# Kernel tuning notes

Measured on AMD Instinct MI355X. Metric: run time of the kernel, lower is better.

Reference implementation:

```python
import jax, jax.numpy as jnp
import numpy as np

B, L, D_IN, D_OUT = 4, 1024, 2048, 2048
H, G = 32, 8            # num_heads, num_kv_groups
HD = D_OUT // H         # head_dim = 64
R = H // G              # group_size = 4


def setup_inputs() -> dict:
    key = jax.random.key(0)
    ks = jax.random.split(key, 7)
    s = 0.02
    return {
        "query": jax.random.normal(ks[0], (B, L, D_IN), jnp.float32),
        "key": jax.random.normal(ks[1], (B, L, D_IN), jnp.float32),
        "value": jax.random.normal(ks[2], (B, L, D_IN), jnp.float32),
        "Wq": jax.random.normal(ks[3], (D_IN, D_OUT), jnp.float32) * s,
        "Wk": jax.random.normal(ks[4], (D_IN, G * HD), jnp.float32) * s,
        "Wv": jax.random.normal(ks[5], (D_IN, G * HD), jnp.float32) * s,
        "Wo": jax.random.normal(ks[6], (D_OUT, D_OUT), jnp.float32) * s,
        # causal mask: positions where mask==True are set to -inf (original uses attn_mask == 1)
        "attn_mask": jnp.triu(jnp.ones((L, L), dtype=bool), k=1),
    }


def reference(query, key, value, Wq, Wk, Wv, Wo, attn_mask):
    b, t, _ = query.shape
    # projections (Linear, no bias)
    q = (query @ Wq).reshape(b, t, G, R, HD)      # head h = g*R + r matches repeat_interleave ordering
    k = (key @ Wk).reshape(b, -1, G, HD)
    v = (value @ Wv).reshape(b, -1, G, HD)
    # NOTE: original code applies NO 1/sqrt(head_dim) scaling — kept faithful.
    # scores: (b, g, r, t, s); KV broadcast over r instead of repeat_interleave
    scores = jnp.einsum('btgrd,bsgd->bgrts', q, k)
    scores = jnp.where(attn_mask[None, None, None, :, :], -jnp.inf, scores)
    weights = jax.nn.softmax(scores, axis=-1)     # dropout p=0.0 -> identity
    ctx = jnp.einsum('bgrts,bsgd->btgrd', weights, v).reshape(b, t, D_OUT)
    attn_output = ctx @ Wo
    attn_output_weights = weights.reshape(b * H, t, -1)  # (b n) t s
    return attn_output, attn_output_weights
```

## Files before the change

### kernel.cpp

```cpp
#include <hip/hip_runtime.h>
#include <math.h>

typedef _Float16 f16;
typedef __attribute__((ext_vector_type(8))) _Float16 f16x8;
typedef __attribute__((ext_vector_type(4))) _Float16 f16x4;
typedef __attribute__((ext_vector_type(4))) float f32x4;
typedef unsigned int u32;

#define MFMA16(a, b, c) __builtin_amdgcn_mfma_f32_16x16x32_f16(a, b, c, 0, 0, 0)

__device__ __forceinline__ void gload16(const void* g, void* l) {
  __builtin_amdgcn_global_load_lds((const __attribute__((address_space(1))) u32*)g,
                                   (__attribute__((address_space(3))) u32*)l, 16, 0, 0);
}

__global__ __launch_bounds__(256) void prep_kernel(
    const float* __restrict__ q, const float* __restrict__ k, const float* __restrict__ v,
    f16* __restrict__ qh, f16* __restrict__ kh, f16* __restrict__ vh,
    const float* __restrict__ Wq, const float* __restrict__ Wk,
    const float* __restrict__ Wv, const float* __restrict__ Wo,
    f16* __restrict__ WqT, f16* __restrict__ WkT,
    f16* __restrict__ WvT, f16* __restrict__ WoT) {
  __shared__ f16 tile[64][66];
  const int bx = blockIdx.x;
  const int t = threadIdx.x;
  if (bx < 24576) {
    const int sel = bx >> 13;
    const float* in = (sel == 0) ? q : (sel == 1) ? k : v;
    f16* out = (sel == 0) ? qh : (sel == 1) ? kh : vh;
    const int i = (bx & 8191) * 1024 + t * 4;
    float4 vv = *(const float4*)(in + i);
    f16x4 h;
    h[0] = (f16)vv.x; h[1] = (f16)vv.y; h[2] = (f16)vv.z; h[3] = (f16)vv.w;
    *(f16x4*)(out + i) = h;
    return;
  }
  int id = bx - 24576;
  const float* in;
  f16* out;
  int K, N;
  if (id < 1024)      { in = Wq; out = WqT; K = 2048; N = 2048; }
  else if (id < 1280) { in = Wk; out = WkT; K = 2048; N = 512;  id -= 1024; }
  else if (id < 1536) { in = Wv; out = WvT; K = 2048; N = 512;  id -= 1280; }
  else                { in = Wo; out = WoT; K = 2048; N = 2048; id -= 1536; }
  const int ntn = N >> 6;
  const int tk = (id / ntn) * 64, tn = (id % ntn) * 64;
#pragma unroll
  for (int i = 0; i < 16; i++) {
    int idx = i * 256 + t;
    int r = idx >> 6, c = idx & 63;
    tile[c][r] = (f16)in[(size_t)(tk + r) * N + tn + c];
  }
  __syncthreads();
#pragma unroll
  for (int i = 0; i < 16; i++) {
    int idx = i * 256 + t;
    int r = idx >> 6, c = idx & 63;
    out[(size_t)(tn + r) * K + tk + c] = tile[r][c];
  }
}

template <bool F32OUT>
__device__ __forceinline__ void gemm_body(const f16* __restrict__ Ap,
                                          const f16* __restrict__ Btp,
                                          void* __restrict__ Cp,
                                          int m0, int n0, int N, int K, int vmode) {
  const int tid = threadIdx.x, lane = tid & 63, wid = tid >> 6;
  const int lg = lane >> 4, lr = lane & 15;
  const int wr = (wid >> 1) << 6, wc = (wid & 1) << 6;
  __shared__ f16 As[2][128 * 64];
  __shared__ f16 Bs[2][128 * 64];
  auto stage = [&](const f16* Gp, f16* Ls, int row0, int k0) {
#pragma unroll
    for (int c = 0; c < 4; c++) {
      int u = c * 256 + tid;
      int row = u >> 3, slot = u & 7;
      int gs = slot ^ (row & 7);
      gload16(Gp + (size_t)(row0 + row) * K + k0 + gs * 8,
              Ls + (c * 256 + wid * 64) * 8);
    }
  };
  f32x4 acc[4][4] = {};
  const int nk = K >> 6;
  stage(Ap, As[0], m0, 0);
  stage(Btp, Bs[0], n0, 0);
  for (int k = 0; k < nk; k++) {
    const int cb = k & 1;
    __builtin_amdgcn_s_barrier();
    __builtin_amdgcn_sched_barrier(0);
    if (k + 1 < nk) {
      stage(Ap, As[cb ^ 1], m0, (k + 1) << 6);
      stage(Btp, Bs[cb ^ 1], n0, (k + 1) << 6);
      __builtin_amdgcn_sched_barrier(0);
      asm volatile("s_waitcnt vmcnt(8)" ::: "memory");
    } else {
      __builtin_amdgcn_sched_barrier(0);
      asm volatile("s_waitcnt vmcnt(0)" ::: "memory");
    }
    __builtin_amdgcn_s_barrier();
    __builtin_amdgcn_sched_barrier(0);
    asm volatile("" ::: "memory");
#pragma unroll
    for (int kk = 0; kk < 2; kk++) {
      f16x8 af[4], bf[4];
#pragma unroll
      for (int i = 0; i < 4; i++) {
        int row = wr + i * 16 + lr;
        int sl = (kk * 4 + lg) ^ (row & 7);
        af[i] = *(const f16x8*)&As[cb][row * 64 + sl * 8];
      }
#pragma unroll
      for (int i = 0; i < 4; i++) {
        int row = wc + i * 16 + lr;
        int sl = (kk * 4 + lg) ^ (row & 7);
        bf[i] = *(const f16x8*)&Bs[cb][row * 64 + sl * 8];
      }
#pragma unroll
      for (int i = 0; i < 4; i++)
#pragma unroll
        for (int j = 0; j < 4; j++)
          acc[i][j] = MFMA16(af[i], bf[j], acc[i][j]);
    }
  }
  if (F32OUT) {
    float* C = (float*)Cp;
#pragma unroll
    for (int i = 0; i < 4; i++)
#pragma unroll
      for (int j = 0; j < 4; j++)
#pragma unroll
        for (int rg = 0; rg < 4; rg++) {
          int row = m0 + wr + i * 16 + lg * 4 + rg;
          int col = n0 + wc + j * 16 + lr;
          C[(size_t)row * N + col] = acc[i][j][rg];
        }
  } else if (vmode) {
    f16* C = (f16*)Cp;
#pragma unroll
    for (int i = 0; i < 4; i++)
#pragma unroll
      for (int j = 0; j < 4; j++)
#pragma unroll
        for (int rg = 0; rg < 4; rg++) {
          int row = m0 + wr + i * 16 + lg * 4 + rg;
          int col = n0 + wc + j * 16 + lr;
          C[((size_t)(row >> 10) * 512 + col) * 1024 + (row & 1023)] = (f16)acc[i][j][rg];
        }
  } else {
    f16* C = (f16*)Cp;
#pragma unroll
    for (int i = 0; i < 4; i++)
#pragma unroll
      for (int j = 0; j < 4; j++)
#pragma unroll
        for (int rg = 0; rg < 4; rg++) {
          int row = m0 + wr + i * 16 + lg * 4 + rg;
          int col = n0 + wc + j * 16 + lr;
          C[(size_t)row * N + col] = (f16)acc[i][j][rg];
        }
  }
}

__global__ __launch_bounds__(256) void gemm_proj(
    const f16* __restrict__ qh, const f16* __restrict__ WqT, f16* __restrict__ Qp,
    const f16* __restrict__ kh, const f16* __restrict__ WkT, f16* __restrict__ Kpj,
    const f16* __restrict__ vh, const f16* __restrict__ WvT, f16* __restrict__ VTp,
    float* __restrict__ wout) {
  const int bx = blockIdx.x;
  const int grp = bx / 5, rem = bx % 5;
  if (rem >= 3) {
    const int zid = grp * 2 + (rem - 3);
#pragma unroll
    for (int ci = 0; ci < 4; ci++) {
      const int c = zid * 4 + ci;
      const int bh = c >> 4, k = c & 15;
      if (k == 15) continue;
      const int cols0 = (k + 1) << 6;
      const int nc4 = (1024 - cols0) >> 2;
      float* base = wout + (size_t)bh * 1024 * 1024 + (size_t)(k << 6) * 1024 + cols0;
      f32x4 z = {};
      for (int r = 0; r < 64; r++) {
        float* rp = base + (size_t)r * 1024;
        for (int c4 = (int)threadIdx.x; c4 < nc4; c4 += 256)
          __builtin_nontemporal_store(z, (f32x4*)(rp + c4 * 4));
      }
    }
    return;
  }
  const int gid = grp * 3 + rem;
  const f16 *Ap, *Btp;
  f16* Cp;
  int N, nsh, vmode, tile;
  if (gid < 512)      { Ap = qh; Btp = WqT; Cp = Qp;  N = 2048; nsh = 4; vmode = 0; tile = gid; }
  else if (gid < 640) { Ap = kh; Btp = WkT; Cp = Kpj; N = 512;  nsh = 2; vmode = 0; tile = gid - 512; }
  else                { Ap = vh; Btp = WvT; Cp = VTp; N = 512;  nsh = 2; vmode = 1; tile = gid - 640; }
  const int m0 = (tile >> nsh) << 7, n0 = (tile & ((1 << nsh) - 1)) << 7;
  gemm_body<false>(Ap, Btp, (void*)Cp, m0, n0, N, 2048, vmode);
}

__global__ __launch_bounds__(256) void gemm_out(
    const f16* __restrict__ Ap, const f16* __restrict__ Btp, float* __restrict__ Cp) {
  const int tile = blockIdx.x;
  const int m0 = (tile >> 4) << 7, n0 = (tile & 15) << 7;
  gemm_body<true>(Ap, Btp, (void*)Cp, m0, n0, 2048, 2048, 0);
}

__global__ __launch_bounds__(256) void attn_kernel(
    const f16* __restrict__ Qp, const f16* __restrict__ Kp, const f16* __restrict__ VTp,
    float* __restrict__ Wout, f16* __restrict__ Ctx) {
  __shared__ f16 Kt[2][64 * 64];
  __shared__ f16 Vt[2][64 * 64];
  __shared__ f16 Wt[4][32 * 64];
  const int bx = (blockIdx.x & 7) * 128 + (blockIdx.x >> 3);
  const int qt = bx & 31, g = (bx >> 5) & 7, b = bx >> 8;
  const int tid = threadIdx.x, lane = tid & 63, wid = tid >> 6;
  const int lg = lane >> 4, lr = lane & 15;
  const int h = g * 4 + wid;
  const int q0 = qt * 32;
  const int st_max = (q0 + 31) >> 6;
  const float S0 = 12.0f;

  f16x8 aq[2][2];
#pragma unroll
  for (int mi = 0; mi < 2; mi++)
#pragma unroll
    for (int kk = 0; kk < 2; kk++)
      aq[mi][kk] = *(const f16x8*)(Qp + (size_t)(b * 1024 + q0 + mi * 16 + lr) * 2048 +
                                   h * 64 + kk * 32 + lg * 8);

  float l_[2][4] = {};

  auto stageK = [&](int st, int buf) {
#pragma unroll
    for (int c = 0; c < 2; c++) {
      int u = c * 256 + tid;
      int row = u >> 3, slot = u & 7;
      int gs = slot ^ (row & 7);
      gload16(Kp + (size_t)(b * 1024 + st * 64 + row) * 512 + g * 64 + gs * 8,
              &Kt[buf][(c * 256 + wid * 64) * 8]);
    }
  };
  auto stageV = [&](int st, int buf) {
#pragma unroll
    for (int c = 0; c < 2; c++) {
      int u = c * 256 + tid;
      int row = u >> 3, slot = u & 7;
      int gs = slot ^ (row & 7);
      gload16(VTp + ((size_t)b * 512 + g * 64 + row) * 1024 + st * 64 + gs * 8,
              &Vt[buf][(c * 256 + wid * 64) * 8]);
    }
  };

  int cur = 0;
  stageK(0, 0);
  for (int st = 0; st <= st_max; st++) {
    __syncthreads();
    if (st < st_max) {
      stageK(st + 1, cur ^ 1);
    } else {
      stageK(0, cur ^ 1);
      stageV(0, cur ^ 1);
    }
    f16x8 bk[4][2];
#pragma unroll
    for (int ni = 0; ni < 4; ni++)
#pragma unroll
      for (int kk = 0; kk < 2; kk++) {
        int row = ni * 16 + lr;
        int sl = (kk * 4 + lg) ^ (row & 7);
        bk[ni][kk] = *(const f16x8*)&Kt[cur][row * 64 + sl * 8];
      }
#pragma unroll
    for (int mi = 0; mi < 2; mi++) {
      f32x4 s[4];
#pragma unroll
      for (int ni = 0; ni < 4; ni++) {
        f32x4 z = {};
        z = MFMA16(aq[mi][0], bk[ni][0], z);
        z = MFMA16(aq[mi][1], bk[ni][1], z);
        s[ni] = z;
      }
      if (st == st_max) {
#pragma unroll
        for (int ni = 0; ni < 4; ni++)
#pragma unroll
          for (int rg = 0; rg < 4; rg++)
            if (st * 64 + ni * 16 + lr > q0 + mi * 16 + lg * 4 + rg) s[ni][rg] = -INFINITY;
      }
#pragma unroll
      for (int rg = 0; rg < 4; rg++) {
        float rs = __expf(s[0][rg] - S0) + __expf(s[1][rg] - S0) +
                   __expf(s[2][rg] - S0) + __expf(s[3][rg] - S0);
        rs += __shfl_xor(rs, 1);
        rs += __shfl_xor(rs, 2);
        rs += __shfl_xor(rs, 4);
        rs += __shfl_xor(rs, 8);
        l_[mi][rg] += rs;
      }
    }
    cur ^= 1;
  }
#pragma unroll
  for (int i = 0; i < 2; i++)
#pragma unroll
    for (int j = 0; j < 4; j++) l_[i][j] = 1.0f / l_[i][j];

  f32x4 o[2][4] = {};
  for (int st = 0; st <= st_max; st++) {
    __syncthreads();
    if (st < st_max) {
      stageK(st + 1, cur ^ 1);
      stageV(st + 1, cur ^ 1);
    }
    f16x8 bk[4][2];
#pragma unroll
    for (int ni = 0; ni < 4; ni++)
#pragma unroll
      for (int kk = 0; kk < 2; kk++) {
        int row = ni * 16 + lr;
        int sl = (kk * 4 + lg) ^ (row & 7);
        bk[ni][kk] = *(const f16x8*)&Kt[cur][row * 64 + sl * 8];
      }
#pragma unroll
    for (int mi = 0; mi < 2; mi++) {
#pragma unroll
      for (int ni = 0; ni < 4; ni++) {
        f32x4 z = {};
        z = MFMA16(aq[mi][0], bk[ni][0], z);
        z = MFMA16(aq[mi][1], bk[ni][1], z);
#pragma unroll
        for (int rg = 0; rg < 4; rg++) {
          float sv = z[rg];
          if (st == st_max && (st * 64 + ni * 16 + lr > q0 + mi * 16 + lg * 4 + rg))
            sv = -INFINITY;
          float w = __expf(sv - S0) * l_[mi][rg];
          int rowl = mi * 16 + lg * 4 + rg;
          __builtin_nontemporal_store(
              w, &Wout[((size_t)(b * 32 + h) * 1024 + q0 + rowl) * 1024 +
                       st * 64 + ni * 16 + lr]);
          int sl2 = (2 * ni + (lr >> 3)) ^ (rowl & 7);
          Wt[wid][rowl * 64 + sl2 * 8 + (lr & 7)] = (f16)w;
        }
      }
    }
#pragma unroll
    for (int kk = 0; kk < 2; kk++) {
      f16x8 aw[2], bv[4];
#pragma unroll
      for (int i = 0; i < 2; i++) {
        int rw = i * 16 + lr;
        int sl = (kk * 4 + lg) ^ (rw & 7);
        aw[i] = *(const f16x8*)&Wt[wid][rw * 64 + sl * 8];
      }
#pragma unroll
      for (int j = 0; j < 4; j++) {
        int rv = j * 16 + lr;
        int sl = (kk * 4 + lg) ^ (rv & 7);
        bv[j] = *(const f16x8*)&Vt[cur][rv * 64 + sl * 8];
      }
#pragma unroll
      for (int i = 0; i < 2; i++)
#pragma unroll
        for (int j = 0; j < 4; j++)
          o[i][j] = MFMA16(aw[i], bv[j], o[i][j]);
    }
    cur ^= 1;
  }

#pragma unroll
  for (int i = 0; i < 2; i++)
#pragma unroll
    for (int j = 0; j < 4; j++)
#pragma unroll
      for (int rg = 0; rg < 4; rg++)
        Ctx[(size_t)(b * 1024 + q0 + i * 16 + lg * 4 + rg) * 2048 +
            h * 64 + j * 16 + lr] = (f16)o[i][j][rg];
}

extern "C" void kernel_launch(void* const* d_in, const int* in_sizes, int n_in,
                              void* d_out, int out_size, void* d_ws, size_t ws_size,
                              hipStream_t stream) {
  const float* query = (const float*)d_in[0];
  const float* key   = (const float*)d_in[1];
  const float* value = (const float*)d_in[2];
  const float* Wq    = (const float*)d_in[3];
  const float* Wk    = (const float*)d_in[4];
  const float* Wv    = (const float*)d_in[5];
  const float* Wo    = (const float*)d_in[6];

  float* out0 = (float*)d_out;
  float* wout = out0 + (size_t)4 * 1024 * 2048;

  char* ws = (char*)d_ws;
  size_t off = 0;
  auto alloc = [&](size_t bytes) {
    char* p = ws + off;
    off += (bytes + 255) & ~(size_t)255;
    return p;
  };
  const size_t NT = 4096;
  f16* qh  = (f16*)alloc(NT * 2048 * 2);
  f16* kh  = (f16*)alloc(NT * 2048 * 2);
  f16* vh  = (f16*)alloc(NT * 2048 * 2);
  f16* WqT = (f16*)alloc((size_t)2048 * 2048 * 2);
  f16* WkT = (f16*)alloc((size_t)512 * 2048 * 2);
  f16* WvT = (f16*)alloc((size_t)512 * 2048 * 2);
  f16* WoT = (f16*)alloc((size_t)2048 * 2048 * 2);
  f16* Qp  = (f16*)alloc(NT * 2048 * 2);
  f16* Kpj = (f16*)alloc(NT * 512 * 2);
  f16* VTp = (f16*)alloc(NT * 512 * 2);
  f16* ctx = (f16*)alloc(NT * 2048 * 2);
  (void)ws_size;

  hipLaunchKernelGGL(prep_kernel, dim3(27136), dim3(256), 0, stream,
                     query, key, value, qh, kh, vh,
                     Wq, Wk, Wv, Wo, WqT, WkT, WvT, WoT);
  hipLaunchKernelGGL(gemm_proj, dim3(1280), dim3(256), 0, stream,
                     qh, WqT, Qp, kh, WkT, Kpj, vh, WvT, VTp, wout);
  hipLaunchKernelGGL(attn_kernel, dim3(1024), dim3(256), 0, stream,
                     Qp, Kpj, VTp, wout, ctx);
  hipLaunchKernelGGL(gemm_out, dim3(512), dim3(256), 0, stream, ctx, WoT, out0);
  (void)in_sizes; (void)n_in; (void)out_size;
}
```

Baseline: 330.2 us.

## Load attention K/V directly from global and shrink GEMM K-tile to 32

The attention kernel drops its LDS double-buffered K and V staging and barriers, and each wave now reads K and V fragments straight from global memory (relying on the cache, since the four waves share the same KV group). The shared GEMM body halves its K step to 32 and removes the XOR swizzle on its LDS tiles, which halves LDS use but doubles the number of barrier iterations. Risks include LDS bank conflicts from the unswizzled tiles, more barrier overhead in the GEMMs, and uncoalesced, repeated global loads in attention.

```diff
diff --git a/kernel.cpp b/kernel.cpp
--- a/kernel.cpp
+++ b/kernel.cpp
@@ -68,20 +68,19 @@
   const int tid = threadIdx.x, lane = tid & 63, wid = tid >> 6;
   const int lg = lane >> 4, lr = lane & 15;
   const int wr = (wid >> 1) << 6, wc = (wid & 1) << 6;
-  __shared__ f16 As[2][128 * 64];
-  __shared__ f16 Bs[2][128 * 64];
+  __shared__ f16 As[2][128 * 32];
+  __shared__ f16 Bs[2][128 * 32];
   auto stage = [&](const f16* Gp, f16* Ls, int row0, int k0) {
 #pragma unroll
-    for (int c = 0; c < 4; c++) {
+    for (int c = 0; c < 2; c++) {
       int u = c * 256 + tid;
-      int row = u >> 3, slot = u & 7;
-      int gs = slot ^ (row & 7);
-      gload16(Gp + (size_t)(row0 + row) * K + k0 + gs * 8,
+      int row = u >> 2, slot = u & 3;
+      gload16(Gp + (size_t)(row0 + row) * K + k0 + slot * 8,
               Ls + (c * 256 + wid * 64) * 8);
     }
   };
   f32x4 acc[4][4] = {};
-  const int nk = K >> 6;
+  const int nk = K >> 5;
   stage(Ap, As[0], m0, 0);
   stage(Btp, Bs[0], n0, 0);
   for (int k = 0; k < nk; k++) {
@@ -89,38 +88,28 @@
     __builtin_amdgcn_s_barrier();
     __builtin_amdgcn_sched_barrier(0);
     if (k + 1 < nk) {
-      stage(Ap, As[cb ^ 1], m0, (k + 1) << 6);
-      stage(Btp, Bs[cb ^ 1], n0, (k + 1) << 6);
+      stage(Ap, As[cb ^ 1], m0, (k + 1) << 5);
+      stage(Btp, Bs[cb ^ 1], n0, (k + 1) << 5);
       __builtin_amdgcn_sched_barrier(0);
-      asm volatile("s_waitcnt vmcnt(8)" ::: "memory");
+      asm volatile("s_waitcnt vmcnt(4)" ::: "memory");
     } else {
       __builtin_amdgcn_sched_barrier(0);
       asm volatile("s_waitcnt vmcnt(0)" ::: "memory");
     }
     __builtin_amdgcn_s_barrier();
     __builtin_amdgcn_sched_barrier(0);
-    asm volatile("" ::: "memory");
-#pragma unroll
-    for (int kk = 0; kk < 2; kk++) {
-      f16x8 af[4], bf[4];
-#pragma unroll
-      for (int i = 0; i < 4; i++) {
-        int row = wr + i * 16 + lr;
-        int sl = (kk * 4 + lg) ^ (row & 7);
-        af[i] = *(const f16x8*)&As[cb][row * 64 + sl * 8];
-      }
-#pragma unroll
-      for (int i = 0; i < 4; i++) {
-        int row = wc + i * 16 + lr;
-        int sl = (kk * 4 + lg) ^ (row & 7);
-        bf[i] = *(const f16x8*)&Bs[cb][row * 64 + sl * 8];
-      }
-#pragma unroll
-      for (int i = 0; i < 4; i++)
-#pragma unroll
-        for (int j = 0; j < 4; j++)
-          acc[i][j] = MFMA16(af[i], bf[j], acc[i][j]);
-    }
+    f16x8 af[4], bf[4];
+#pragma unroll
+    for (int i = 0; i < 4; i++)
+      af[i] = *(const f16x8*)&As[cb][(wr + i * 16 + lr) * 32 + lg * 8];
+#pragma unroll
+    for (int i = 0; i < 4; i++)
+      bf[i] = *(const f16x8*)&Bs[cb][(wc + i * 16 + lr) * 32 + lg * 8];
+#pragma unroll
+    for (int i = 0; i < 4; i++)
+#pragma unroll
+      for (int j = 0; j < 4; j++)
+        acc[i][j] = MFMA16(af[i], bf[j], acc[i][j]);
   }
   if (F32OUT) {
     float* C = (float*)Cp;
@@ -208,8 +197,6 @@
 __global__ __launch_bounds__(256) void attn_kernel(
     const f16* __restrict__ Qp, const f16* __restrict__ Kp, const f16* __restrict__ VTp,
     float* __restrict__ Wout, f16* __restrict__ Ctx) {
-  __shared__ f16 Kt[2][64 * 64];
-  __shared__ f16 Vt[2][64 * 64];
   __shared__ f16 Wt[4][32 * 64];
   const int bx = (blockIdx.x & 7) * 128 + (blockIdx.x >> 3);
   const int qt = bx & 31, g = (bx >> 5) & 7, b = bx >> 8;
@@ -220,6 +207,9 @@
   const int st_max = (q0 + 31) >> 6;
   const float S0 = 12.0f;
 
+  const f16* Kb = Kp + (size_t)b * 1024 * 512 + g * 64;
+  const f16* Vb = VTp + ((size_t)b * 512 + g * 64) * 1024;
+
   f16x8 aq[2][2];
 #pragma unroll
   for (int mi = 0; mi < 2; mi++)
@@ -230,46 +220,14 @@
 
   float l_[2][4] = {};
 
-  auto stageK = [&](int st, int buf) {
-#pragma unroll
-    for (int c = 0; c < 2; c++) {
-      int u = c * 256 + tid;
-      int row = u >> 3, slot = u & 7;
-      int gs = slot ^ (row & 7);
-      gload16(Kp + (size_t)(b * 1024 + st * 64 + row) * 512 + g * 64 + gs * 8,
-              &Kt[buf][(c * 256 + wid * 64) * 8]);
-    }
-  };
-  auto stageV = [&](int st, int buf) {
-#pragma unroll
-    for (int c = 0; c < 2; c++) {
-      int u = c * 256 + tid;
-      int row = u >> 3, slot = u & 7;
-      int gs = slot ^ (row & 7);
-      gload16(VTp + ((size_t)b * 512 + g * 64 + row) * 1024 + st * 64 + gs * 8,
-              &Vt[buf][(c * 256 + wid * 64) * 8]);
-    }
-  };
-
-  int cur = 0;
-  stageK(0, 0);
   for (int st = 0; st <= st_max; st++) {
-    __syncthreads();
-    if (st < st_max) {
-      stageK(st + 1, cur ^ 1);
-    } else {
-      stageK(0, cur ^ 1);
-      stageV(0, cur ^ 1);
-    }
     f16x8 bk[4][2];
 #pragma unroll
     for (int ni = 0; ni < 4; ni++)
 #pragma unroll
-      for (int kk = 0; kk < 2; kk++) {
-        int row = ni * 16 + lr;
-        int sl = (kk * 4 + lg) ^ (row & 7);
-        bk[ni][kk] = *(const f16x8*)&Kt[cur][row * 64 + sl * 8];
-      }
+      for (int kk = 0; kk < 2; kk++)
+        bk[ni][kk] = *(const f16x8*)(Kb + (size_t)(st * 64 + ni * 16 + lr) * 512 +
+                                     kk * 32 + lg * 8);
 #pragma unroll
     for (int mi = 0; mi < 2; mi++) {
       f32x4 s[4];
@@ -298,7 +256,6 @@
         l_[mi][rg] += rs;
       }
     }
-    cur ^= 1;
   }
 #pragma unroll
   for (int i = 0; i < 2; i++)
@@ -307,20 +264,13 @@
 
   f32x4 o[2][4] = {};
   for (int st = 0; st <= st_max; st++) {
-    __syncthreads();
-    if (st < st_max) {
-      stageK(st + 1, cur ^ 1);
-      stageV(st + 1, cur ^ 1);
-    }
     f16x8 bk[4][2];
 #pragma unroll
     for (int ni = 0; ni < 4; ni++)
 #pragma unroll
-      for (int kk = 0; kk < 2; kk++) {
-        int row = ni * 16 + lr;
-        int sl = (kk * 4 + lg) ^ (row & 7);
-        bk[ni][kk] = *(const f16x8*)&Kt[cur][row * 64 + sl * 8];
-      }
+      for (int kk = 0; kk < 2; kk++)
+        bk[ni][kk] = *(const f16x8*)(Kb + (size_t)(st * 64 + ni * 16 + lr) * 512 +
+                                     kk * 32 + lg * 8);
 #pragma unroll
     for (int mi = 0; mi < 2; mi++) {
 #pragma unroll
@@ -353,18 +303,15 @@
         aw[i] = *(const f16x8*)&Wt[wid][rw * 64 + sl * 8];
       }
 #pragma unroll
-      for (int j = 0; j < 4; j++) {
-        int rv = j * 16 + lr;
-        int sl = (kk * 4 + lg) ^ (rv & 7);
-        bv[j] = *(const f16x8*)&Vt[cur][rv * 64 + sl * 8];
-      }
+      for (int j = 0; j < 4; j++)
+        bv[j] = *(const f16x8*)(Vb + (size_t)(j * 16 + lr) * 1024 +
+                                st * 64 + kk * 32 + lg * 8);
 #pragma unroll
       for (int i = 0; i < 2; i++)
 #pragma unroll
         for (int j = 0; j < 4; j++)
           o[i][j] = MFMA16(aw[i], bv[j], o[i][j]);
     }
-    cur ^= 1;
   }
 
 #pragma unroll
```

Result: slower. 396.3 us (+20.0%).

## Move Wo transpose into projection kernel and swizzle block order for XCD locality

Applied to the files above, without the earlier changes.

Moves the Wo fp32-to-fp16 transpose out of the prep kernel and into extra blocks of the projection GEMM launch, so it overlaps with the GEMM work instead of adding to the prep phase. Block indices in gemm_proj and gemm_out are remapped so consecutive tiles land on the same XCD, aiming for better L2 reuse. The fp32 output GEMM now uses nontemporal stores. In exchange, gemm_proj gets a larger grid and a shared-memory tile, which may reduce its occupancy.

```diff
diff --git a/kernel.cpp b/kernel.cpp
--- a/kernel.cpp
+++ b/kernel.cpp
@@ -18,9 +18,8 @@
     const float* __restrict__ q, const float* __restrict__ k, const float* __restrict__ v,
     f16* __restrict__ qh, f16* __restrict__ kh, f16* __restrict__ vh,
     const float* __restrict__ Wq, const float* __restrict__ Wk,
-    const float* __restrict__ Wv, const float* __restrict__ Wo,
-    f16* __restrict__ WqT, f16* __restrict__ WkT,
-    f16* __restrict__ WvT, f16* __restrict__ WoT) {
+    const float* __restrict__ Wv,
+    f16* __restrict__ WqT, f16* __restrict__ WkT, f16* __restrict__ WvT) {
   __shared__ f16 tile[64][66];
   const int bx = blockIdx.x;
   const int t = threadIdx.x;
@@ -41,8 +40,7 @@
   int K, N;
   if (id < 1024)      { in = Wq; out = WqT; K = 2048; N = 2048; }
   else if (id < 1280) { in = Wk; out = WkT; K = 2048; N = 512;  id -= 1024; }
-  else if (id < 1536) { in = Wv; out = WvT; K = 2048; N = 512;  id -= 1280; }
-  else                { in = Wo; out = WoT; K = 2048; N = 2048; id -= 1536; }
+  else                { in = Wv; out = WvT; K = 2048; N = 512;  id -= 1280; }
   const int ntn = N >> 6;
   const int tk = (id / ntn) * 64, tn = (id % ntn) * 64;
 #pragma unroll
@@ -132,7 +130,7 @@
         for (int rg = 0; rg < 4; rg++) {
           int row = m0 + wr + i * 16 + lg * 4 + rg;
           int col = n0 + wc + j * 16 + lr;
-          C[(size_t)row * N + col] = acc[i][j][rg];
+          __builtin_nontemporal_store(acc[i][j][rg], &C[(size_t)row * N + col]);
         }
   } else if (vmode) {
     f16* C = (f16*)Cp;
@@ -165,9 +163,29 @@
     const f16* __restrict__ qh, const f16* __restrict__ WqT, f16* __restrict__ Qp,
     const f16* __restrict__ kh, const f16* __restrict__ WkT, f16* __restrict__ Kpj,
     const f16* __restrict__ vh, const f16* __restrict__ WvT, f16* __restrict__ VTp,
-    float* __restrict__ wout) {
-  const int bx = blockIdx.x;
-  const int grp = bx / 5, rem = bx % 5;
+    float* __restrict__ wout, const float* __restrict__ Wo, f16* __restrict__ WoT) {
+  __shared__ f16 ttile[64][66];
+  const int bxs = (blockIdx.x & 7) * 288 + (blockIdx.x >> 3);
+  if (bxs >= 1280) {
+    const int id = bxs - 1280;
+    const int tk = (id >> 5) * 64, tn = (id & 31) * 64;
+    const int t = threadIdx.x;
+#pragma unroll
+    for (int i = 0; i < 16; i++) {
+      int idx = i * 256 + t;
+      int r = idx >> 6, c = idx & 63;
+      ttile[c][r] = (f16)Wo[(size_t)(tk + r) * 2048 + tn + c];
+    }
+    __syncthreads();
+#pragma unroll
+    for (int i = 0; i < 16; i++) {
+      int idx = i * 256 + t;
+      int r = idx >> 6, c = idx & 63;
+      WoT[(size_t)(tn + r) * 2048 + tk + c] = ttile[r][c];
+    }
+    return;
+  }
+  const int grp = bxs / 5, rem = bxs % 5;
   if (rem >= 3) {
     const int zid = grp * 2 + (rem - 3);
 #pragma unroll
@@ -200,7 +218,7 @@
 
 __global__ __launch_bounds__(256) void gemm_out(
     const f16* __restrict__ Ap, const f16* __restrict__ Btp, float* __restrict__ Cp) {
-  const int tile = blockIdx.x;
+  const int tile = (blockIdx.x & 7) * 64 + (blockIdx.x >> 3);
   const int m0 = (tile >> 4) << 7, n0 = (tile & 15) << 7;
   gemm_body<true>(Ap, Btp, (void*)Cp, m0, n0, 2048, 2048, 0);
 }
@@ -412,11 +430,11 @@
   f16* ctx = (f16*)alloc(NT * 2048 * 2);
   (void)ws_size;
 
-  hipLaunchKernelGGL(prep_kernel, dim3(27136), dim3(256), 0, stream,
+  hipLaunchKernelGGL(prep_kernel, dim3(26112), dim3(256), 0, stream,
                      query, key, value, qh, kh, vh,
-                     Wq, Wk, Wv, Wo, WqT, WkT, WvT, WoT);
-  hipLaunchKernelGGL(gemm_proj, dim3(1280), dim3(256), 0, stream,
-                     qh, WqT, Qp, kh, WkT, Kpj, vh, WvT, VTp, wout);
+                     Wq, Wk, Wv, WqT, WkT, WvT);
+  hipLaunchKernelGGL(gemm_proj, dim3(2304), dim3(256), 0, stream,
+                     qh, WqT, Qp, kh, WkT, Kpj, vh, WvT, VTp, wout, Wo, WoT);
   hipLaunchKernelGGL(attn_kernel, dim3(1024), dim3(256), 0, stream,
                      Qp, Kpj, VTp, wout, ctx);
   hipLaunchKernelGGL(gemm_out, dim3(512), dim3(256), 0, stream, ctx, WoT, out0);
```

After: 358.2 us. 8.5% more time.
